# Performance work log

Hardware: AMD Instinct MI355X
Metric: run time of the kernel (lower is better)

The kernel has to match this reference:

```python
import jax, jax.numpy as jnp
import numpy as np

E, H, L = 512, 1024, 4
VS, VT = 32000, 32000
B, SS, TT = 64, 48, 48
PAD = 0


def _cell(x, h, c, Wih, Whh, bih, bhh):
    # torch.nn.LSTMCell math: gate order i, f, g, o
    g = x @ Wih.T + h @ Whh.T + bih + bhh
    i, f, gg, o = jnp.split(g, 4, axis=-1)
    c = jax.nn.sigmoid(f) * c + jax.nn.sigmoid(i) * jnp.tanh(gg)
    h = jax.nn.sigmoid(o) * jnp.tanh(c)
    return h, c


def setup_inputs() -> dict:
    key = jax.random.key(0)
    ks = jax.random.split(key, 14)
    s = 0.05
    d = {}
    d['src_tokens'] = jax.random.randint(ks[0], (SS, B), 0, VS, dtype=jnp.int32)
    d['tgt_tokens'] = jax.random.randint(ks[1], (TT, B), 0, VT, dtype=jnp.int32)
    d['src_emb'] = jax.random.normal(ks[2], (VS, E)) * s
    d['tgt_emb'] = jax.random.normal(ks[3], (VT, E)) * s
    d['enc_Wih0'] = jax.random.normal(ks[4], (4 * H, E)) * s
    d['enc_WihR'] = jax.random.normal(ks[5], (L - 1, 4 * H, H)) * s
    d['enc_Whh'] = jax.random.normal(ks[6], (L, 4 * H, H)) * s
    d['enc_bih'] = jnp.zeros((L, 4 * H))
    d['enc_bhh'] = jnp.zeros((L, 4 * H))
    d['dec_Wih0'] = jax.random.normal(ks[7], (4 * H, E + H)) * s
    d['dec_WihR'] = jax.random.normal(ks[8], (L - 1, 4 * H, H)) * s
    d['dec_Whh'] = jax.random.normal(ks[9], (L, 4 * H, H)) * s
    d['dec_bih'] = jnp.zeros((L, 4 * H))
    d['dec_bhh'] = jnp.zeros((L, 4 * H))
    d['att_vec_W'] = jax.random.normal(ks[10], (H, 2 * H)) * s
    d['readout_W'] = jax.random.normal(ks[11], (VT, H)) * s
    return d


def _forward(src_tokens, tgt_tokens, src_emb, tgt_emb, enc_Wih0, enc_WihR,
             enc_Whh, enc_bih, enc_bhh, dec_Wih0, dec_WihR, dec_Whh, dec_bih,
             dec_bhh, att_vec_W, readout_W):
    src_x = src_emb[src_tokens]                      # [SS, B, E]
    h0 = jnp.zeros((L, B, H), src_emb.dtype)
    c0 = jnp.zeros((L, B, H), src_emb.dtype)

    def enc_step(carry, x_t):
        h, c = carry
        inp = x_t
        hs, cs = [], []
        for l in range(L):
            Wih = enc_Wih0 if l == 0 else enc_WihR[l - 1]
            hn, cn = _cell(inp, h[l], c[l], Wih, enc_Whh[l], enc_bih[l], enc_bhh[l])
            hs.append(hn); cs.append(cn)
            inp = hn
        return (jnp.stack(hs), jnp.stack(cs)), inp

    (hT, cT), enc_out = jax.lax.scan(enc_step, (h0, c0), src_x)
    src_enc = enc_out.transpose(1, 0, 2)             # [B, SS, H]

    # decoder init: last encoder layer (h, c) copied to every decoder layer
    hd = jnp.tile(hT[-1][None], (L, 1, 1))
    cd = jnp.tile(cT[-1][None], (L, 1, 1))
    tgt_x = tgt_emb[tgt_tokens[:-1]]                 # [TT-1, B, E]
    att0 = jnp.zeros((B, H), src_emb.dtype)

    def dec_step(carry, y_t):
        h, c, att = carry
        inp = jnp.concatenate([y_t, att], axis=-1)   # input feeding
        hs, cs = [], []
        for l in range(L):
            Wih = dec_Wih0 if l == 0 else dec_WihR[l - 1]
            hn, cn = _cell(inp, h[l], c[l], Wih, dec_Whh[l], dec_bih[l], dec_bhh[l])
            hs.append(hn); cs.append(cn)
            inp = hn
        h_top = hs[-1]
        # global attention, 'dot' score (full-length seqs -> all-zero mask is a no-op)
        scores = jnp.einsum('bsh,bh->bs', src_enc, h_top)
        alpha = jax.nn.softmax(scores, axis=-1)
        ctx = jnp.einsum('bs,bsh->bh', alpha, src_enc)
        att_t = jnp.tanh(jnp.concatenate([h_top, ctx], axis=-1) @ att_vec_W.T)
        return (jnp.stack(hs), jnp.stack(cs), att_t), att_t

    _, att_ves = jax.lax.scan(dec_step, (hd, cd, att0), tgt_x)  # [TT-1, B, H]

    logp = jax.nn.log_softmax(att_ves @ readout_W.T, axis=-1)   # [TT-1, B, VT]
    gold = tgt_tokens[1:]
    gold_lp = jnp.take_along_axis(logp, gold[..., None], axis=-1)[..., 0]
    mask = (gold != PAD).astype(logp.dtype)
    return (gold_lp * mask).sum(axis=0)              # [B]


def reference(src_tokens, tgt_tokens, src_emb, tgt_emb, enc_Wih0, enc_WihR,
              enc_Whh, enc_bih, enc_bhh, dec_Wih0, dec_WihR, dec_Whh, dec_bih,
              dec_bhh, att_vec_W, readout_W):
    return _forward(src_tokens, tgt_tokens, src_emb, tgt_emb, enc_Wih0,
                    enc_WihR, enc_Whh, enc_bih, enc_bhh, dec_Wih0, dec_WihR,
                    dec_Whh, dec_bih, dec_bhh, att_vec_W, readout_W)
```

## Files before the change

### kernel.cpp

```cpp
#include <hip/hip_runtime.h>


typedef __attribute__((ext_vector_type(8))) short bf16x8;
typedef __attribute__((ext_vector_type(4))) float f32x4;

#define SMEM_G  49152
#define SMEM_A  65536
#define SMEM_R  40960

#define NMT_SYNC_LIGHT()                                   \
  do {                                                     \
    asm volatile("s_waitcnt lgkmcnt(0)" ::: "memory");     \
    __builtin_amdgcn_s_barrier();                          \
    __builtin_amdgcn_sched_barrier(0);                     \
  } while (0)

__device__ __forceinline__ float bf2f(ushort u) {
  union { uint i; float f; } v; v.i = ((uint)u) << 16; return v.f;
}
__device__ __forceinline__ ushort f2bf(float x) {
  union { float f; uint i; } v; v.f = x;
  uint r = (v.i + 0x7fffu + ((v.i >> 16) & 1u)) >> 16;
  return (ushort)r;
}
__device__ __forceinline__ uint pack2(float x, float y) {
  return (uint)f2bf(x) | ((uint)f2bf(y) << 16);
}
__device__ __forceinline__ float sigm(float x) {
  return __fdividef(1.f, 1.f + __expf(-x));
}
__device__ __forceinline__ float tanhf_fast(float x) {
  const float e = __expf(2.f * x);
  return 1.f - __fdividef(2.f, e + 1.f);
}

__device__ __forceinline__ void gemm_term(
    const ushort* __restrict__ A, int lda,
    const ushort* __restrict__ W, int ldw,
    int K, int m0, int n0,
    f32x4 acc[4], char* s)
{
  const int tid = threadIdx.x;
  const int lane = tid & 63;
  const int w = tid >> 6;
  const int r0 = tid >> 3;
  const int cge = (tid & 7) << 3;
  const int so0 = r0 * 128 + (((tid & 7) << 4) ^ ((r0 & 7) << 4));
  const ushort* Ar0 = A + (size_t)(m0 + r0) * lda + cge;
  const ushort* Ar1 = A + (size_t)(m0 + r0 + 32) * lda + cge;
  const ushort* Wr0 = W + (size_t)(n0 + r0) * ldw + cge;
  const ushort* Wr1 = W + (size_t)(n0 + r0 + 32) * ldw + cge;
  const int NT = K >> 6;

  uint4 a0s0, a1s0, b0s0, b1s0;
  uint4 a0s1, a1s1, b0s1, b1s1;
  uint4 a0s2, a1s2, b0s2, b1s2;

  a0s0 = *(const uint4*)(Ar0);       a1s0 = *(const uint4*)(Ar1);
  b0s0 = *(const uint4*)(Wr0);       b1s0 = *(const uint4*)(Wr1);
  a0s1 = *(const uint4*)(Ar0 + 64);  a1s1 = *(const uint4*)(Ar1 + 64);
  b0s1 = *(const uint4*)(Wr0 + 64);  b1s1 = *(const uint4*)(Wr1 + 64);
  a0s2 = *(const uint4*)(Ar0 + 128); a1s2 = *(const uint4*)(Ar1 + 128);
  b0s2 = *(const uint4*)(Wr0 + 128); b1s2 = *(const uint4*)(Wr1 + 128);
  {
    char* sl = s;
    *(uint4*)(sl + so0) = a0s0;         *(uint4*)(sl + 4096 + so0) = a1s0;
    *(uint4*)(sl + 8192 + so0) = b0s0;  *(uint4*)(sl + 12288 + so0) = b1s0;
    sl = s + 16384;
    *(uint4*)(sl + so0) = a0s1;         *(uint4*)(sl + 4096 + so0) = a1s1;
    *(uint4*)(sl + 8192 + so0) = b0s1;  *(uint4*)(sl + 12288 + so0) = b1s1;
  }
  if (3 < NT) {
    a0s0 = *(const uint4*)(Ar0 + 192); a1s0 = *(const uint4*)(Ar1 + 192);
    b0s0 = *(const uint4*)(Wr0 + 192); b1s0 = *(const uint4*)(Wr1 + 192);
  }
  if (4 < NT) {
    a0s1 = *(const uint4*)(Ar0 + 256); a1s1 = *(const uint4*)(Ar1 + 256);
    b0s1 = *(const uint4*)(Wr0 + 256); b1s1 = *(const uint4*)(Wr1 + 256);
  }

  const int axor = (lane & 7) << 4;
  const int arow = (w * 16 + (lane & 15)) * 128;
  const int brow = (lane & 15) * 128;
  const int kb0 = (lane >> 4) << 4;

#define NMT_ROUND(KR, CUR, ST)                                                \
  do {                                                                        \
    NMT_SYNC_LIGHT();                                                         \
    if ((KR) + 2 < NT) {                                                      \
      char* sl_ = s + (ST) * 16384;                                           \
      *(uint4*)(sl_ + so0) = a0s##ST;                                         \
      *(uint4*)(sl_ + 4096 + so0) = a1s##ST;                                  \
      *(uint4*)(sl_ + 8192 + so0) = b0s##ST;                                  \
      *(uint4*)(sl_ + 12288 + so0) = b1s##ST;                                 \
      if ((KR) + 5 < NT) {                                                    \
        const int off_ = ((KR) + 5) << 6;                                     \
        a0s##ST = *(const uint4*)(Ar0 + off_);                                \
        a1s##ST = *(const uint4*)(Ar1 + off_);                                \
        b0s##ST = *(const uint4*)(Wr0 + off_);                                \
        b1s##ST = *(const uint4*)(Wr1 + off_);                                \
      }                                                                       \
    }                                                                         \
    char* cur_ = s + (CUR) * 16384;                                           \
    _Pragma("unroll")                                                         \
    for (int ks = 0; ks < 2; ++ks) {                                          \
      const int kb = (ks << 6) + kb0;                                         \
      bf16x8 af = *(const bf16x8*)(cur_ + arow + (kb ^ axor));                \
      _Pragma("unroll")                                                       \
      for (int nf = 0; nf < 4; ++nf) {                                        \
        bf16x8 bfr = *(const bf16x8*)(cur_ + 8192 + nf * 2048 + brow +        \
                                      (kb ^ axor));                           \
        acc[nf] = __builtin_amdgcn_mfma_f32_16x16x32_bf16(af, bfr, acc[nf],   \
                                                          0, 0, 0);           \
      }                                                                       \
    }                                                                         \
  } while (0)

  for (int kb_ = 0; kb_ < NT; kb_ += 3) {
    NMT_ROUND(kb_ + 0, 0, 2);
    if (kb_ + 1 < NT) NMT_ROUND(kb_ + 1, 1, 0);
    if (kb_ + 2 < NT) NMT_ROUND(kb_ + 2, 2, 1);
  }
#undef NMT_ROUND
  __syncthreads();
}

__device__ __forceinline__ void att_loadf(
    const float* H0, const float* H1, const float* C0, const float* C1,
    int kt, float4* fh, float4* fc)
{
#pragma unroll
  for (int q = 0; q < 8; ++q) {
    const int rh = q >> 2, sub = (q >> 1) & 1, vq = q & 1;
    const float* hp_ = rh ? H1 : H0;
    const float* cp_ = rh ? C1 : C0;
    fh[q] = *reinterpret_cast<const float4*>(hp_ + kt + sub * 64 + vq * 4);
    fc[q] = *reinterpret_cast<const float4*>(cp_ + kt + sub * 64 + vq * 4);
  }
}

__device__ __forceinline__ void att_store(
    char* buf, int soX, const float4* fh, const float4* fc)
{
#pragma unroll
  for (int rh = 0; rh < 2; ++rh)
#pragma unroll
    for (int sub = 0; sub < 2; ++sub) {
      const int q0 = rh * 4 + sub * 2;
      const float4 u = fh[q0], v = fc[q0];
      const float4 u2 = fh[q0 + 1], v2 = fc[q0 + 1];
      uint4 o;
      o.x = pack2(tanhf_fast(u.x + v.x), tanhf_fast(u.y + v.y));
      o.y = pack2(tanhf_fast(u.z + v.z), tanhf_fast(u.w + v.w));
      o.z = pack2(tanhf_fast(u2.x + v2.x), tanhf_fast(u2.y + v2.y));
      o.w = pack2(tanhf_fast(u2.z + v2.z), tanhf_fast(u2.w + v2.w));
      *reinterpret_cast<uint4*>(buf + sub * 8192 + rh * 4096 + soX) = o;
    }
}

__device__ __forceinline__ void gemm_att(
    const float* __restrict__ H, const float* __restrict__ C2,
    const ushort* __restrict__ W, int ldw, int n0,
    f32x4 acc[4], char* s)
{
  char* sA0 = s;
  char* sB0 = s + 16384;
  char* sA1 = s + 32768;
  char* sB1 = s + 49152;
  const int tid = threadIdx.x;
  const int lane = tid & 63;
  const int w = tid >> 6;
  const int r0 = tid >> 3;
  const int cge = (tid & 7) << 3;
  const int soX = r0 * 128 + (((tid & 7) << 4) ^ ((r0 & 7) << 4));
  const ushort* Wr0 = W + (size_t)(n0 + r0) * ldw + cge;
  const ushort* Wr1 = W + (size_t)(n0 + r0 + 32) * ldw + cge;
  const float* H0 = H + r0 * 1024 + cge;
  const float* H1 = H + (r0 + 32) * 1024 + cge;
  const float* C0 = C2 + r0 * 1024 + cge;
  const float* C1 = C2 + (r0 + 32) * 1024 + cge;

  float4 fh[8], fc[8];
  uint4 b0, b1, b2, b3;
  att_loadf(H0, H1, C0, C1, 0, fh, fc);
  att_store(sA0, soX, fh, fc);
  b0 = *reinterpret_cast<const uint4*>(Wr0);
  b1 = *reinterpret_cast<const uint4*>(Wr1);
  b2 = *reinterpret_cast<const uint4*>(Wr0 + 64);
  b3 = *reinterpret_cast<const uint4*>(Wr1 + 64);
  *reinterpret_cast<uint4*>(sB0 + soX) = b0;
  *reinterpret_cast<uint4*>(sB0 + 4096 + soX) = b1;
  *reinterpret_cast<uint4*>(sB0 + 8192 + soX) = b2;
  *reinterpret_cast<uint4*>(sB0 + 12288 + soX) = b3;
  att_loadf(H0, H1, C0, C1, 128, fh, fc);
  b0 = *reinterpret_cast<const uint4*>(Wr0 + 128);
  b1 = *reinterpret_cast<const uint4*>(Wr1 + 128);
  b2 = *reinterpret_cast<const uint4*>(Wr0 + 192);
  b3 = *reinterpret_cast<const uint4*>(Wr1 + 192);

  const int axor = (lane & 7) << 4;
  const int arow = (w * 16 + (lane & 15)) * 128;
  const int brow = (lane & 15) * 128;
  const int kb0 = (lane >> 4) << 4;
  for (int kt = 0; kt < 1024; kt += 128) {
    char* cA = (kt & 128) ? sA1 : sA0;
    char* cB = (kt & 128) ? sB1 : sB0;
    char* nA = (kt & 128) ? sA0 : sA1;
    char* nB = (kt & 128) ? sB0 : sB1;
    NMT_SYNC_LIGHT();
    if (kt + 128 < 1024) {
      att_store(nA, soX, fh, fc);
      *reinterpret_cast<uint4*>(nB + soX) = b0;
      *reinterpret_cast<uint4*>(nB + 4096 + soX) = b1;
      *reinterpret_cast<uint4*>(nB + 8192 + soX) = b2;
      *reinterpret_cast<uint4*>(nB + 12288 + soX) = b3;
      if (kt + 256 < 1024) {
        att_loadf(H0, H1, C0, C1, kt + 256, fh, fc);
        b0 = *reinterpret_cast<const uint4*>(Wr0 + kt + 256);
        b1 = *reinterpret_cast<const uint4*>(Wr1 + kt + 256);
        b2 = *reinterpret_cast<const uint4*>(Wr0 + kt + 320);
        b3 = *reinterpret_cast<const uint4*>(Wr1 + kt + 320);
      }
    }
#pragma unroll
    for (int ks = 0; ks < 4; ++ks) {
      const int sb = (ks >> 1) * 8192;
      const int kb = ((ks & 1) << 6) + kb0;
      bf16x8 af = *reinterpret_cast<const bf16x8*>(cA + sb + arow + (kb ^ axor));
#pragma unroll
      for (int nf = 0; nf < 4; ++nf) {
        bf16x8 bfr = *reinterpret_cast<const bf16x8*>(
            cB + sb + nf * 2048 + brow + (kb ^ axor));
        acc[nf] = __builtin_amdgcn_mfma_f32_16x16x32_bf16(af, bfr, acc[nf], 0, 0, 0);
      }
    }
  }
  __syncthreads();
}

__device__ __forceinline__ void store_f32(
    float* __restrict__ out, int ldo, int m0, int n0, f32x4 acc[4])
{
  const int tid = threadIdx.x, lane = tid & 63, w = tid >> 6;
  const int rbase = w * 16 + ((lane >> 4) << 2);
  const int cb = lane & 15;
#pragma unroll
  for (int nf = 0; nf < 4; ++nf)
#pragma unroll
    for (int r = 0; r < 4; ++r)
      out[(size_t)(m0 + rbase + r) * ldo + n0 + nf * 16 + cb] = acc[nf][r];
}

__device__ __forceinline__ void cell_store(
    float* smemF, f32x4 acc[4],
    float* __restrict__ c, ushort* __restrict__ hout,
    ushort* __restrict__ senc_t, int j0)
{
  const int tid = threadIdx.x, lane = tid & 63, w = tid >> 6;
  const int rbase = w * 16 + ((lane >> 4) << 2);
  const int cb = lane & 15;
  __syncthreads();
#pragma unroll
  for (int nf = 0; nf < 4; ++nf)
#pragma unroll
    for (int r = 0; r < 4; ++r)
      smemF[(rbase + r) * 68 + nf * 16 + cb] = acc[nf][r];
  __syncthreads();
#pragma unroll
  for (int i = 0; i < 4; ++i) {
    const int id = tid + i * 256;
    const int b = id >> 4, u = id & 15;
    const float g0 = smemF[b * 68 + u * 4 + 0];
    const float g1 = smemF[b * 68 + u * 4 + 1];
    const float g2 = smemF[b * 68 + u * 4 + 2];
    const float g3 = smemF[b * 68 + u * 4 + 3];
    const int off = b * 1024 + j0 + u;
    const float cold = c[off];
    const float cn = sigm(g1) * cold + sigm(g0) * tanhf_fast(g2);
    const float hv = sigm(g3) * tanhf_fast(cn);
    c[off] = cn;
    const ushort hb = f2bf(hv);
    hout[off] = hb;
    if (senc_t) senc_t[(size_t)b * 49152 + j0 + u] = hb;
  }
}

__global__ __launch_bounds__(256) void nmt_init(
    float* c, ushort* henc, float* hbAll, float* ctxAll)
{
  const int idx = blockIdx.x * 256 + threadIdx.x;
  if (idx < 262144) c[idx] = 0.f;
  if (idx < 65536) {
    hbAll[idx] = 0.f;
    ctxAll[idx] = 0.f;
    henc[idx] = 0;
    henc[(size_t)1 * 49 * 65536 + idx] = 0;
    henc[(size_t)2 * 49 * 65536 + idx] = 0;
    henc[(size_t)3 * 49 * 65536 + idx] = 0;
  }
}

__global__ __launch_bounds__(256) void nmt_convperm(
    const float* __restrict__ in, ushort* __restrict__ out,
    int L, int Kin, int col0, int Kout)
{
  const size_t idx = (size_t)blockIdx.x * 256 + threadIdx.x;
  const size_t total = (size_t)L * 4096 * Kout;
  if (idx >= total) return;
  const int k = (int)(idx % Kout);
  const size_t rem = idx / Kout;
  const int rp = (int)(rem % 4096);
  const int l = (int)(rem / 4096);
  const int j = rp >> 2, g = rp & 3;
  out[idx] = f2bf(in[((size_t)l * 4096 + g * 1024 + j) * Kin + col0 + k]);
}

__global__ __launch_bounds__(256) void nmt_convplain(
    const float* __restrict__ in, ushort* __restrict__ out, size_t n)
{
  const size_t idx = (size_t)blockIdx.x * 256 + threadIdx.x;
  if (idx < n) out[idx] = f2bf(in[idx]);
}

__global__ __launch_bounds__(256) void nmt_bias(
    const float* __restrict__ bih, const float* __restrict__ bhh, float* __restrict__ bc)
{
  const int idx = blockIdx.x * 256 + threadIdx.x;
  if (idx >= 4 * 4096) return;
  const int rp = idx & 4095, l = idx >> 12;
  const int j = rp >> 2, g = rp & 3;
  bc[idx] = bih[l * 4096 + g * 1024 + j] + bhh[l * 4096 + g * 1024 + j];
}

__global__ __launch_bounds__(256) void nmt_gather(
    const int* __restrict__ tok, const float* __restrict__ emb,
    ushort* __restrict__ out, int rows)
{
  const size_t idx = (size_t)blockIdx.x * 256 + threadIdx.x;
  if (idx >= (size_t)rows * 512) return;
  const int k = (int)(idx & 511);
  const int r = (int)(idx >> 9);
  out[idx] = f2bf(emb[(size_t)tok[r] * 512 + k]);
}

__global__ __launch_bounds__(256) void nmt_pre(
    const ushort* __restrict__ A, const ushort* __restrict__ Wp,
    const float* __restrict__ bc0, float* __restrict__ out, int K)
{
  __shared__ __align__(16) char smem[SMEM_G];
  const int m0 = blockIdx.x * 64, n0 = blockIdx.y * 64;
  const int lane = threadIdx.x & 63;
  const int cb = lane & 15;
  f32x4 acc[4];
#pragma unroll
  for (int nf = 0; nf < 4; ++nf) {
    const float bv = bc0[n0 + nf * 16 + cb];
#pragma unroll
    for (int r = 0; r < 4; ++r) acc[nf][r] = bv;
  }
  gemm_term(A, K, Wp, K, K, m0, n0, acc, smem);
  store_f32(out, 4096, m0, n0, acc);
}

__global__ __launch_bounds__(256) void nmt_decinit(
    const ushort* __restrict__ henc, float* c, ushort* h)
{
  const int idx = blockIdx.x * 256 + threadIdx.x;
  if (idx >= 65536) return;
  const ushort hv = henc[((size_t)3 * 49 + 48) * 65536 + idx];
  const float cv = c[3 * 65536 + idx];
  c[idx] = cv; c[65536 + idx] = cv; c[2 * 65536 + idx] = cv;
  h[idx] = hv; h[65536 + idx] = hv; h[2 * 65536 + idx] = hv; h[3 * 65536 + idx] = hv;
}

__global__ __launch_bounds__(256) void nmt_sv(
    const ushort* __restrict__ senc, const ushort* __restrict__ attW,
    ushort* __restrict__ SV)
{
  __shared__ __align__(16) char smem[SMEM_G];
  const int b = blockIdx.x;
  const int n0 = blockIdx.y * 64;
  const int tid = threadIdx.x, lane = tid & 63, w = tid >> 6;
  const int rbase = w * 16 + ((lane >> 4) << 2), cb = lane & 15;
  f32x4 acc[4];
#pragma unroll
  for (int nf = 0; nf < 4; ++nf)
#pragma unroll
    for (int r = 0; r < 4; ++r) acc[nf][r] = 0.f;
  gemm_term(senc + (size_t)b * 49152, 1024, attW + 1024, 2048, 1024, 0, n0,
            acc, smem);
#pragma unroll
  for (int nf = 0; nf < 4; ++nf)
#pragma unroll
    for (int r = 0; r < 4; ++r) {
      const int row = rbase + r;
      if (row < 48)
        SV[(size_t)b * 49152 + row * 1024 + n0 + nf * 16 + cb] = f2bf(acc[nf][r]);
    }
}

__global__ __launch_bounds__(256) void nmt_enc_cell(
    int u, int lo, ushort* __restrict__ henc, ushort* __restrict__ srcenc,
    float* __restrict__ c,
    const ushort* __restrict__ WihR, const ushort* __restrict__ Whh,
    const float* __restrict__ X0, const float* __restrict__ bcE)
{
  __shared__ __align__(16) char smem[SMEM_G];
  const int l = lo + blockIdx.y;
  const int t = u - l;
  const int n0 = blockIdx.x * 64;
  const int tid = threadIdx.x, lane = tid & 63, w = tid >> 6;
  const int rbase = w * 16 + ((lane >> 4) << 2), cb = lane & 15;
  f32x4 acc[4];
  if (l == 0) {
#pragma unroll
    for (int nf = 0; nf < 4; ++nf)
#pragma unroll
      for (int r = 0; r < 4; ++r)
        acc[nf][r] = X0[(size_t)t * 262144 + (size_t)(rbase + r) * 4096 + n0 + nf * 16 + cb];
  } else {
#pragma unroll
    for (int nf = 0; nf < 4; ++nf) {
      const float bv = bcE[l * 4096 + n0 + nf * 16 + cb];
#pragma unroll
      for (int r = 0; r < 4; ++r) acc[nf][r] = bv;
    }
    gemm_term(henc + ((size_t)(l - 1) * 49 + t + 1) * 65536, 1024,
              WihR + (size_t)(l - 1) * 4194304, 1024, 1024, 0, n0, acc, smem);
  }
  gemm_term(henc + ((size_t)l * 49 + t) * 65536, 1024,
            Whh + (size_t)l * 4194304, 1024, 1024, 0, n0, acc, smem);
  cell_store((float*)smem, acc, c + l * 65536,
             henc + ((size_t)l * 49 + t + 1) * 65536,
             (l == 3) ? (srcenc + t * 1024) : (ushort*)nullptr, n0 >> 2);
}

__global__ __launch_bounds__(256) void nmt_dec_stage(
    int l, const ushort* __restrict__ hp, ushort* __restrict__ hn,
    float* __restrict__ c,
    const ushort* __restrict__ Whh, const ushort* __restrict__ WihR,
    const ushort* __restrict__ Wd0a,
    const float* __restrict__ hbprev, const float* __restrict__ ctxprev,
    const float* __restrict__ Y0t, const float* __restrict__ bcD,
    float* __restrict__ pbuf)
{
  __shared__ __align__(16) char smem[SMEM_A];
  const int n0 = blockIdx.x * 64;
  const int tid = threadIdx.x, lane = tid & 63, w = tid >> 6;
  const int rbase = w * 16 + ((lane >> 4) << 2), cb = lane & 15;
  f32x4 acc[4];
  if (blockIdx.y == 0) {
    if (l == 0) {
#pragma unroll
      for (int nf = 0; nf < 4; ++nf)
#pragma unroll
        for (int r = 0; r < 4; ++r) {
          const size_t o = (size_t)(rbase + r) * 4096 + n0 + nf * 16 + cb;
          acc[nf][r] = Y0t[o] + pbuf[o];
        }
      gemm_att(hbprev, ctxprev, Wd0a, 1024, n0, acc, smem);
    } else {
#pragma unroll
      for (int nf = 0; nf < 4; ++nf)
#pragma unroll
        for (int r = 0; r < 4; ++r)
          acc[nf][r] = pbuf[(size_t)l * 262144 + (size_t)(rbase + r) * 4096 + n0 + nf * 16 + cb];
      gemm_term(hn + (l - 1) * 65536, 1024, WihR + (size_t)(l - 1) * 4194304,
                1024, 1024, 0, n0, acc, smem);
    }
    cell_store((float*)smem, acc, c + l * 65536, hn + l * 65536,
               (ushort*)nullptr, n0 >> 2);
  } else {
    const int lp = (l + 1) & 3;
    if (lp == 0) {
#pragma unroll
      for (int nf = 0; nf < 4; ++nf)
#pragma unroll
        for (int r = 0; r < 4; ++r) acc[nf][r] = 0.f;
      gemm_term(hn, 1024, Whh, 1024, 1024, 0, n0, acc, smem);
    } else {
#pragma unroll
      for (int nf = 0; nf < 4; ++nf) {
        const float bv = bcD[lp * 4096 + n0 + nf * 16 + cb];
#pragma unroll
        for (int r = 0; r < 4; ++r) acc[nf][r] = bv;
      }
      gemm_term(hp + lp * 65536, 1024, Whh + (size_t)lp * 4194304,
                1024, 1024, 0, n0, acc, smem);
    }
    store_f32(pbuf + (size_t)lp * 262144, 4096, 0, n0, acc);
  }
}

__global__ __launch_bounds__(256) void nmt_partial0(
    const ushort* __restrict__ h0, const ushort* __restrict__ Whh0,
    float* __restrict__ pbuf)
{
  __shared__ __align__(16) char smem[SMEM_G];
  const int n0 = blockIdx.x * 64;
  f32x4 acc[4];
#pragma unroll
  for (int nf = 0; nf < 4; ++nf)
#pragma unroll
    for (int r = 0; r < 4; ++r) acc[nf][r] = 0.f;
  gemm_term(h0, 1024, Whh0, 1024, 1024, 0, n0, acc, smem);
  store_f32(pbuf, 4096, 0, n0, acc);
}

__global__ __launch_bounds__(256) void nmt_attnAB(
    const ushort* __restrict__ h3, const ushort* __restrict__ senc,
    const ushort* __restrict__ SV, const ushort* __restrict__ attW,
    float* __restrict__ ctx2, float* __restrict__ hb)
{
  __shared__ __align__(16) char smem[SMEM_G];
  const int bid = blockIdx.x;
  const int tid = threadIdx.x, lane = tid & 63, w = tid >> 6;
  if (bid < 64) {
    float* sc = (float*)smem;
    float* al = (float*)smem + 64;
    const int b = bid;
    const ushort* sb = senc + (size_t)b * 49152;
    const ushort* vb = SV + (size_t)b * 49152;
    float hreg[16];
#pragma unroll
    for (int q = 0; q < 16; ++q) hreg[q] = bf2f(h3[b * 1024 + lane * 16 + q]);
    for (int s = w; s < 48; s += 4) {
      const ushort* vr = sb + s * 1024 + lane * 16;
      float p = 0.f;
#pragma unroll
      for (int q = 0; q < 16; ++q) p += bf2f(vr[q]) * hreg[q];
      for (int d = 1; d < 64; d <<= 1) p += __shfl_xor(p, d);
      if (lane == 0) sc[s] = p;
    }
    __syncthreads();
    if (tid < 64) {
      const float v = (lane < 48) ? sc[lane] : -3.4e38f;
      float m = v;
      for (int d = 1; d < 64; d <<= 1) m = fmaxf(m, __shfl_xor(m, d));
      float e = (lane < 48) ? expf(v - m) : 0.f;
      float s = e;
      for (int d = 1; d < 64; d <<= 1) s += __shfl_xor(s, d);
      al[lane] = e / s;
    }
    __syncthreads();
    const int k0 = tid * 4;
    float a0 = 0, a1 = 0, a2 = 0, a3 = 0;
    for (int s = 0; s < 48; ++s) {
      const float als = al[s];
      const ushort* vr = vb + s * 1024 + k0;
      a0 += als * bf2f(vr[0]); a1 += als * bf2f(vr[1]);
      a2 += als * bf2f(vr[2]); a3 += als * bf2f(vr[3]);
    }
    ctx2[b * 1024 + k0 + 0] = a0; ctx2[b * 1024 + k0 + 1] = a1;
    ctx2[b * 1024 + k0 + 2] = a2; ctx2[b * 1024 + k0 + 3] = a3;
  } else {
    const int n0 = (bid - 64) * 64;
    f32x4 acc[4];
#pragma unroll
    for (int nf = 0; nf < 4; ++nf)
#pragma unroll
      for (int r = 0; r < 4; ++r) acc[nf][r] = 0.f;
    gemm_term(h3, 1024, attW, 2048, 1024, 0, n0, acc, smem);
    store_f32(hb, 1024, 0, n0, acc);
  }
}

__global__ __launch_bounds__(256) void nmt_attves_k(
    const float* __restrict__ hbAll, const float* __restrict__ ctxAll,
    ushort* __restrict__ attves)
{
  const int i = blockIdx.x * 1024 + threadIdx.x * 4;
#pragma unroll
  for (int k = 0; k < 4; ++k) {
    const int j = i + k;
    attves[j] = f2bf(tanhf_fast(hbAll[j + 65536] + ctxAll[j + 65536]));
  }
}

__global__ __launch_bounds__(256) void nmt_readout(
    const ushort* __restrict__ attves, const ushort* __restrict__ routW,
    const int* __restrict__ tgt, float* __restrict__ pmax,
    float* __restrict__ psum, float* __restrict__ goldl)
{
  __shared__ __align__(16) char smem[SMEM_R];
  const int g = blockIdx.x;
  const int n0 = blockIdx.y * 64;
  const int tid = threadIdx.x, lane = tid & 63, w = tid >> 6;
  const int rbase = w * 16 + ((lane >> 4) << 2), cb = lane & 15;
  const int r0 = tid >> 3;
  const int cge = (tid & 7) << 3;
  const int soX = r0 * 128 + (((tid & 7) << 4) ^ ((r0 & 7) << 4));
  const int axor = (lane & 7) << 4;
  const int arow = (w * 16 + (lane & 15)) * 128;
  const int brow = (lane & 15) * 128;
  const int kb0 = (lane >> 4) << 4;

  f32x4 acc[4][4];
#pragma unroll
  for (int mi = 0; mi < 4; ++mi)
#pragma unroll
    for (int nf = 0; nf < 4; ++nf)
#pragma unroll
      for (int r = 0; r < 4; ++r) acc[mi][nf][r] = 0.f;

  for (int kt = 0; kt < 1024; kt += 64) {
    __syncthreads();
#pragma unroll
    for (int mi = 0; mi < 4; ++mi) {
      const size_t mr = (size_t)(g * 256 + mi * 64 + r0) * 1024 + kt + cge;
      *(uint4*)(smem + mi * 8192 + soX) = *(const uint4*)(attves + mr);
      *(uint4*)(smem + mi * 8192 + 4096 + soX) = *(const uint4*)(attves + mr + 32 * 1024);
    }
    {
      const size_t wr = (size_t)(n0 + r0) * 1024 + kt + cge;
      *(uint4*)(smem + 32768 + soX) = *(const uint4*)(routW + wr);
      *(uint4*)(smem + 32768 + 4096 + soX) = *(const uint4*)(routW + wr + 32 * 1024);
    }
    __syncthreads();
#pragma unroll
    for (int ks = 0; ks < 2; ++ks) {
      const int kb = (ks << 6) + kb0;
      bf16x8 bf0 = *(const bf16x8*)(smem + 32768 + 0 * 2048 + brow + (kb ^ axor));
      bf16x8 bf1 = *(const bf16x8*)(smem + 32768 + 1 * 2048 + brow + (kb ^ axor));
      bf16x8 bf2 = *(const bf16x8*)(smem + 32768 + 2 * 2048 + brow + (kb ^ axor));
      bf16x8 bf3 = *(const bf16x8*)(smem + 32768 + 3 * 2048 + brow + (kb ^ axor));
#pragma unroll
      for (int mi = 0; mi < 4; ++mi) {
        bf16x8 af = *(const bf16x8*)(smem + mi * 8192 + arow + (kb ^ axor));
        acc[mi][0] = __builtin_amdgcn_mfma_f32_16x16x32_bf16(af, bf0, acc[mi][0], 0, 0, 0);
        acc[mi][1] = __builtin_amdgcn_mfma_f32_16x16x32_bf16(af, bf1, acc[mi][1], 0, 0, 0);
        acc[mi][2] = __builtin_amdgcn_mfma_f32_16x16x32_bf16(af, bf2, acc[mi][2], 0, 0, 0);
        acc[mi][3] = __builtin_amdgcn_mfma_f32_16x16x32_bf16(af, bf3, acc[mi][3], 0, 0, 0);
      }
    }
  }

#pragma unroll
  for (int mi = 0; mi < 4; ++mi) {
    const int gm = g * 4 + mi;
    if (gm >= 47) continue;
#pragma unroll
    for (int r = 0; r < 4; ++r) {
      float lm = fmaxf(fmaxf(acc[mi][0][r], acc[mi][1][r]),
                       fmaxf(acc[mi][2][r], acc[mi][3][r]));
      for (int d = 1; d < 16; d <<= 1) lm = fmaxf(lm, __shfl_xor(lm, d));
      float ls = 0.f;
#pragma unroll
      for (int nf = 0; nf < 4; ++nf) ls += expf(acc[mi][nf][r] - lm);
      for (int d = 1; d < 16; d <<= 1) ls += __shfl_xor(ls, d);
      const int grow = gm * 64 + rbase + r;
      if (cb == 0) {
        pmax[(size_t)grow * 500 + blockIdx.y] = lm;
        psum[(size_t)grow * 500 + blockIdx.y] = ls;
      }
      const int t = grow >> 6, b = grow & 63;
      const int gold = tgt[(t + 1) * 64 + b];
#pragma unroll
      for (int nf = 0; nf < 4; ++nf)
        if (n0 + nf * 16 + cb == gold) goldl[grow] = acc[mi][nf][r];
    }
  }
}

__global__ __launch_bounds__(64) void nmt_combine(
    const float* __restrict__ pmax, const float* __restrict__ psum,
    const float* __restrict__ goldl, const int* __restrict__ tgt,
    float* __restrict__ lpm)
{
  const int row = blockIdx.x;
  const int lane = threadIdx.x;
  float m = -3.4e38f, s = 0.f;
  for (int i = lane; i < 500; i += 64) {
    const float pm = pmax[(size_t)row * 500 + i];
    const float ps = psum[(size_t)row * 500 + i];
    if (pm > m) { s = s * expf(m - pm) + ps; m = pm; }
    else        { s += ps * expf(pm - m); }
  }
  for (int d = 1; d < 64; d <<= 1) {
    const float om = __shfl_xor(m, d), os = __shfl_xor(s, d);
    if (om > m) { s = s * expf(m - om) + os; m = om; }
    else        { s += os * expf(om - m); }
  }
  if (lane == 0) {
    const int t = row >> 6, b = row & 63;
    const int gold = tgt[(t + 1) * 64 + b];
    const float lp = goldl[row] - m - logf(s);
    lpm[row] = (gold != 0) ? lp : 0.f;
  }
}

__global__ __launch_bounds__(64) void nmt_final(
    const float* __restrict__ lpm, float* __restrict__ out)
{
  const int b = threadIdx.x;
  float s = 0.f;
  for (int t = 0; t < 47; ++t) s += lpm[t * 64 + b];
  out[b] = s;
}

extern "C" void kernel_launch(void* const* d_in, const int* in_sizes, int n_in,
                              void* d_out, int out_size, void* d_ws, size_t ws_size,
                              hipStream_t stream)
{
  (void)in_sizes; (void)n_in; (void)out_size; (void)ws_size;
  const int*   src_tok  = (const int*)d_in[0];
  const int*   tgt_tok  = (const int*)d_in[1];
  const float* src_emb  = (const float*)d_in[2];
  const float* tgt_emb  = (const float*)d_in[3];
  const float* eWih0    = (const float*)d_in[4];
  const float* eWihR    = (const float*)d_in[5];
  const float* eWhh     = (const float*)d_in[6];
  const float* ebih     = (const float*)d_in[7];
  const float* ebhh     = (const float*)d_in[8];
  const float* dWih0    = (const float*)d_in[9];
  const float* dWihR    = (const float*)d_in[10];
  const float* dWhh     = (const float*)d_in[11];
  const float* dbih     = (const float*)d_in[12];
  const float* dbhh     = (const float*)d_in[13];
  const float* attW_f   = (const float*)d_in[14];
  const float* routW_f  = (const float*)d_in[15];

  char* p = (char*)d_ws;
  auto alloc = [&](size_t bytes) { void* r = (void*)p; p += (bytes + 255) & ~(size_t)255; return r; };
  ushort* eWih0p = (ushort*)alloc((size_t)4096 * 512 * 2);
  ushort* eWihRp = (ushort*)alloc((size_t)3 * 4096 * 1024 * 2);
  ushort* eWhhp  = (ushort*)alloc((size_t)4 * 4096 * 1024 * 2);
  ushort* dWih0y = (ushort*)alloc((size_t)4096 * 512 * 2);
  ushort* dWih0a = (ushort*)alloc((size_t)4096 * 1024 * 2);
  ushort* dWihRp = (ushort*)alloc((size_t)3 * 4096 * 1024 * 2);
  ushort* dWhhp  = (ushort*)alloc((size_t)4 * 4096 * 1024 * 2);
  ushort* attWb  = (ushort*)alloc((size_t)1024 * 2048 * 2);
  ushort* routWb = (ushort*)alloc((size_t)32000 * 1024 * 2);
  ushort* srcx   = (ushort*)alloc((size_t)3072 * 512 * 2);
  ushort* tgtx   = (ushort*)alloc((size_t)3008 * 512 * 2);
  ushort* henc   = (ushort*)alloc((size_t)4 * 49 * 65536 * 2);
  ushort* hA     = (ushort*)alloc((size_t)4 * 65536 * 2);
  ushort* hB     = (ushort*)alloc((size_t)4 * 65536 * 2);
  ushort* srcenc = (ushort*)alloc((size_t)64 * 49152 * 2);
  ushort* SVbuf  = (ushort*)alloc((size_t)64 * 49152 * 2);
  ushort* attves = (ushort*)alloc((size_t)3072 * 1024 * 2);
  float*  hbAll  = (float*)alloc((size_t)48 * 65536 * 4);
  float*  ctxAll = (float*)alloc((size_t)48 * 65536 * 4);
  float*  pbuf   = (float*)alloc((size_t)4 * 262144 * 4);
  float*  X0     = (float*)alloc((size_t)3072 * 4096 * 4);
  float*  Y0     = (float*)alloc((size_t)3008 * 4096 * 4);
  float*  bcE    = (float*)alloc((size_t)16384 * 4);
  float*  bcD    = (float*)alloc((size_t)16384 * 4);
  float*  cbuf   = (float*)alloc((size_t)4 * 65536 * 4);
  float*  pmaxb  = (float*)alloc((size_t)3008 * 500 * 4);
  float*  psumb  = (float*)alloc((size_t)3008 * 500 * 4);
  float*  goldl  = (float*)alloc((size_t)3008 * 4);
  float*  lpm    = (float*)alloc((size_t)3008 * 4);

  const dim3 B256(256);
  auto g1 = [](size_t n) { return dim3((unsigned)((n + 255) / 256)); };

  nmt_init<<<g1(262144), B256, 0, stream>>>(cbuf, henc, hbAll, ctxAll);

  nmt_convperm<<<g1((size_t)4096 * 512), B256, 0, stream>>>(eWih0, eWih0p, 1, 512, 0, 512);
  nmt_convperm<<<g1((size_t)3 * 4096 * 1024), B256, 0, stream>>>(eWihR, eWihRp, 3, 1024, 0, 1024);
  nmt_convperm<<<g1((size_t)4 * 4096 * 1024), B256, 0, stream>>>(eWhh, eWhhp, 4, 1024, 0, 1024);
  nmt_convperm<<<g1((size_t)4096 * 512), B256, 0, stream>>>(dWih0, dWih0y, 1, 1536, 0, 512);
  nmt_convperm<<<g1((size_t)4096 * 1024), B256, 0, stream>>>(dWih0, dWih0a, 1, 1536, 512, 1024);
  nmt_convperm<<<g1((size_t)3 * 4096 * 1024), B256, 0, stream>>>(dWihR, dWihRp, 3, 1024, 0, 1024);
  nmt_convperm<<<g1((size_t)4 * 4096 * 1024), B256, 0, stream>>>(dWhh, dWhhp, 4, 1024, 0, 1024);
  nmt_convplain<<<g1((size_t)1024 * 2048), B256, 0, stream>>>(attW_f, attWb, (size_t)1024 * 2048);
  nmt_convplain<<<g1((size_t)32000 * 1024), B256, 0, stream>>>(routW_f, routWb, (size_t)32000 * 1024);
  nmt_bias<<<g1(16384), B256, 0, stream>>>(ebih, ebhh, bcE);
  nmt_bias<<<g1(16384), B256, 0, stream>>>(dbih, dbhh, bcD);
  nmt_gather<<<g1((size_t)3072 * 512), B256, 0, stream>>>(src_tok, src_emb, srcx, 3072);
  nmt_gather<<<g1((size_t)3008 * 512), B256, 0, stream>>>(tgt_tok, tgt_emb, tgtx, 3008);

  nmt_pre<<<dim3(48, 64), B256, 0, stream>>>(srcx, eWih0p, bcE, X0, 512);
  nmt_pre<<<dim3(47, 64), B256, 0, stream>>>(tgtx, dWih0y, bcD, Y0, 512);

  for (int u = 0; u < 51; ++u) {
    const int lo = (u > 47) ? (u - 47) : 0;
    const int hi = (u < 3) ? u : 3;
    nmt_enc_cell<<<dim3(64, hi - lo + 1), B256, 0, stream>>>(
        u, lo, henc, srcenc, cbuf, eWihRp, eWhhp, X0, bcE);
  }
  nmt_decinit<<<g1(65536), B256, 0, stream>>>(henc, cbuf, hA);
  nmt_sv<<<dim3(64, 16), B256, 0, stream>>>(srcenc, attWb, SVbuf);
  nmt_partial0<<<dim3(64), B256, 0, stream>>>(hA, dWhhp, pbuf);

  for (int t = 0; t < 47; ++t) {
    ushort* hp = (t & 1) ? hB : hA;
    ushort* hn = (t & 1) ? hA : hB;
    for (int l = 0; l < 4; ++l) {
      nmt_dec_stage<<<dim3(64, 2), B256, 0, stream>>>(
          l, hp, hn, cbuf, dWhhp, dWihRp, dWih0a,
          hbAll + (size_t)t * 65536, ctxAll + (size_t)t * 65536,
          Y0 + (size_t)t * 262144, bcD, pbuf);
    }
    nmt_attnAB<<<dim3(80), B256, 0, stream>>>(
        hn + 3 * 65536, srcenc, SVbuf, attWb,
        ctxAll + (size_t)(t + 1) * 65536, hbAll + (size_t)(t + 1) * 65536);
  }
  nmt_attves_k<<<dim3(3008), B256, 0, stream>>>(hbAll, ctxAll, attves);

  nmt_readout<<<dim3(12, 500), B256, 0, stream>>>(attves, routWb, tgt_tok,
                                                  pmaxb, psumb, goldl);
  nmt_combine<<<dim3(3008), dim3(64), 0, stream>>>(pmaxb, psumb, goldl, tgt_tok, lpm);
  nmt_final<<<dim3(1), dim3(64), 0, stream>>>(lpm, (float*)d_out);
}
```

Before: 4.498 ms.

## Split encoder cell into pipelined input/recurrent halves and enlarge readout M tile

The encoder wavefront is restructured so each layer's input-projection GEMM (WihR·h_below) runs one tick ahead as a separate block set, writing partial sums to a new buffer. The cell blocks then only do the recurrent Whh GEMM plus the cell update, which shortens each launch's critical path at the cost of more ticks (54 instead of 51) and extra fp32 partial-sum traffic. Separately, the readout GEMM tile doubles along M (8 row groups per block, 6 instead of 12 blocks in x) to reuse each loaded weight tile across more rows. This raises shared memory to 72KB and doubles the accumulator registers, which may lower occupancy.

```diff
diff --git a/kernel.cpp b/kernel.cpp
--- a/kernel.cpp
+++ b/kernel.cpp
@@ -6,7 +6,7 @@
 
 #define SMEM_G  49152
 #define SMEM_A  65536
-#define SMEM_R  40960
+#define SMEM_R  73728
 
 #define NMT_SYNC_LIGHT()                                   \
   do {                                                     \
@@ -399,40 +399,53 @@
     }
 }
 
-__global__ __launch_bounds__(256) void nmt_enc_cell(
-    int u, int lo, ushort* __restrict__ henc, ushort* __restrict__ srcenc,
+__global__ __launch_bounds__(256) void nmt_enc_tick(
+    int v, int lc0, int ncell, int lp0,
+    ushort* __restrict__ henc, ushort* __restrict__ srcenc,
     float* __restrict__ c,
     const ushort* __restrict__ WihR, const ushort* __restrict__ Whh,
-    const float* __restrict__ X0, const float* __restrict__ bcE)
+    const float* __restrict__ X0, const float* __restrict__ bcE,
+    float* __restrict__ pbufE)
 {
   __shared__ __align__(16) char smem[SMEM_G];
-  const int l = lo + blockIdx.y;
-  const int t = u - l;
   const int n0 = blockIdx.x * 64;
   const int tid = threadIdx.x, lane = tid & 63, w = tid >> 6;
   const int rbase = w * 16 + ((lane >> 4) << 2), cb = lane & 15;
   f32x4 acc[4];
-  if (l == 0) {
-#pragma unroll
-    for (int nf = 0; nf < 4; ++nf)
-#pragma unroll
-      for (int r = 0; r < 4; ++r)
-        acc[nf][r] = X0[(size_t)t * 262144 + (size_t)(rbase + r) * 4096 + n0 + nf * 16 + cb];
+  if ((int)blockIdx.y < ncell) {
+    const int l = lc0 + blockIdx.y;
+    const int t = v - 2 * l;
+    if (l == 0) {
+#pragma unroll
+      for (int nf = 0; nf < 4; ++nf)
+#pragma unroll
+        for (int r = 0; r < 4; ++r)
+          acc[nf][r] = X0[(size_t)t * 262144 + (size_t)(rbase + r) * 4096 + n0 + nf * 16 + cb];
+    } else {
+#pragma unroll
+      for (int nf = 0; nf < 4; ++nf)
+#pragma unroll
+        for (int r = 0; r < 4; ++r)
+          acc[nf][r] = pbufE[(size_t)l * 262144 + (size_t)(rbase + r) * 4096 + n0 + nf * 16 + cb];
+    }
+    gemm_term(henc + ((size_t)l * 49 + t) * 65536, 1024,
+              Whh + (size_t)l * 4194304, 1024, 1024, 0, n0, acc, smem);
+    cell_store((float*)smem, acc, c + l * 65536,
+               henc + ((size_t)l * 49 + t + 1) * 65536,
+               (l == 3) ? (srcenc + t * 1024) : (ushort*)nullptr, n0 >> 2);
   } else {
+    const int l = lp0 + (blockIdx.y - ncell);
+    const int tp = v + 1 - 2 * l;
 #pragma unroll
     for (int nf = 0; nf < 4; ++nf) {
       const float bv = bcE[l * 4096 + n0 + nf * 16 + cb];
 #pragma unroll
       for (int r = 0; r < 4; ++r) acc[nf][r] = bv;
     }
-    gemm_term(henc + ((size_t)(l - 1) * 49 + t + 1) * 65536, 1024,
+    gemm_term(henc + ((size_t)(l - 1) * 49 + tp + 1) * 65536, 1024,
               WihR + (size_t)(l - 1) * 4194304, 1024, 1024, 0, n0, acc, smem);
-  }
-  gemm_term(henc + ((size_t)l * 49 + t) * 65536, 1024,
-            Whh + (size_t)l * 4194304, 1024, 1024, 0, n0, acc, smem);
-  cell_store((float*)smem, acc, c + l * 65536,
-             henc + ((size_t)l * 49 + t + 1) * 65536,
-             (l == 3) ? (srcenc + t * 1024) : (ushort*)nullptr, n0 >> 2);
+    store_f32(pbufE + (size_t)l * 262144, 4096, 0, n0, acc);
+  }
 }
 
 __global__ __launch_bounds__(256) void nmt_dec_stage(
@@ -595,9 +608,9 @@
   const int brow = (lane & 15) * 128;
   const int kb0 = (lane >> 4) << 4;
 
-  f32x4 acc[4][4];
-#pragma unroll
-  for (int mi = 0; mi < 4; ++mi)
+  f32x4 acc[8][4];
+#pragma unroll
+  for (int mi = 0; mi < 8; ++mi)
 #pragma unroll
     for (int nf = 0; nf < 4; ++nf)
 #pragma unroll
@@ -606,26 +619,26 @@
   for (int kt = 0; kt < 1024; kt += 64) {
     __syncthreads();
 #pragma unroll
-    for (int mi = 0; mi < 4; ++mi) {
-      const size_t mr = (size_t)(g * 256 + mi * 64 + r0) * 1024 + kt + cge;
+    for (int mi = 0; mi < 8; ++mi) {
+      const size_t mr = (size_t)(g * 512 + mi * 64 + r0) * 1024 + kt + cge;
       *(uint4*)(smem + mi * 8192 + soX) = *(const uint4*)(attves + mr);
       *(uint4*)(smem + mi * 8192 + 4096 + soX) = *(const uint4*)(attves + mr + 32 * 1024);
     }
     {
       const size_t wr = (size_t)(n0 + r0) * 1024 + kt + cge;
-      *(uint4*)(smem + 32768 + soX) = *(const uint4*)(routW + wr);
-      *(uint4*)(smem + 32768 + 4096 + soX) = *(const uint4*)(routW + wr + 32 * 1024);
+      *(uint4*)(smem + 65536 + soX) = *(const uint4*)(routW + wr);
+      *(uint4*)(smem + 65536 + 4096 + soX) = *(const uint4*)(routW + wr + 32 * 1024);
     }
     __syncthreads();
 #pragma unroll
     for (int ks = 0; ks < 2; ++ks) {
       const int kb = (ks << 6) + kb0;
-      bf16x8 bf0 = *(const bf16x8*)(smem + 32768 + 0 * 2048 + brow + (kb ^ axor));
-      bf16x8 bf1 = *(const bf16x8*)(smem + 32768 + 1 * 2048 + brow + (kb ^ axor));
-      bf16x8 bf2 = *(const bf16x8*)(smem + 32768 + 2 * 2048 + brow + (kb ^ axor));
-      bf16x8 bf3 = *(const bf16x8*)(smem + 32768 + 3 * 2048 + brow + (kb ^ axor));
-#pragma unroll
-      for (int mi = 0; mi < 4; ++mi) {
+      bf16x8 bf0 = *(const bf16x8*)(smem + 65536 + 0 * 2048 + brow + (kb ^ axor));
+      bf16x8 bf1 = *(const bf16x8*)(smem + 65536 + 1 * 2048 + brow + (kb ^ axor));
+      bf16x8 bf2 = *(const bf16x8*)(smem + 65536 + 2 * 2048 + brow + (kb ^ axor));
+      bf16x8 bf3 = *(const bf16x8*)(smem + 65536 + 3 * 2048 + brow + (kb ^ axor));
+#pragma unroll
+      for (int mi = 0; mi < 8; ++mi) {
         bf16x8 af = *(const bf16x8*)(smem + mi * 8192 + arow + (kb ^ axor));
         acc[mi][0] = __builtin_amdgcn_mfma_f32_16x16x32_bf16(af, bf0, acc[mi][0], 0, 0, 0);
         acc[mi][1] = __builtin_amdgcn_mfma_f32_16x16x32_bf16(af, bf1, acc[mi][1], 0, 0, 0);
@@ -636,8 +649,8 @@
   }
 
 #pragma unroll
-  for (int mi = 0; mi < 4; ++mi) {
-    const int gm = g * 4 + mi;
+  for (int mi = 0; mi < 8; ++mi) {
+    const int gm = g * 8 + mi;
     if (gm >= 47) continue;
 #pragma unroll
     for (int r = 0; r < 4; ++r) {
@@ -742,6 +755,7 @@
   float*  hbAll  = (float*)alloc((size_t)48 * 65536 * 4);
   float*  ctxAll = (float*)alloc((size_t)48 * 65536 * 4);
   float*  pbuf   = (float*)alloc((size_t)4 * 262144 * 4);
+  float*  pbufE  = (float*)alloc((size_t)4 * 262144 * 4);
   float*  X0     = (float*)alloc((size_t)3072 * 4096 * 4);
   float*  Y0     = (float*)alloc((size_t)3008 * 4096 * 4);
   float*  bcE    = (float*)alloc((size_t)16384 * 4);
@@ -774,11 +788,16 @@
   nmt_pre<<<dim3(48, 64), B256, 0, stream>>>(srcx, eWih0p, bcE, X0, 512);
   nmt_pre<<<dim3(47, 64), B256, 0, stream>>>(tgtx, dWih0y, bcD, Y0, 512);
 
-  for (int u = 0; u < 51; ++u) {
-    const int lo = (u > 47) ? (u - 47) : 0;
-    const int hi = (u < 3) ? u : 3;
-    nmt_enc_cell<<<dim3(64, hi - lo + 1), B256, 0, stream>>>(
-        u, lo, henc, srcenc, cbuf, eWihRp, eWhhp, X0, bcE);
+  for (int v = 0; v < 54; ++v) {
+    int lc0 = (v > 47) ? ((v - 47 + 1) / 2) : 0;
+    int lc1 = (v / 2 < 3) ? (v / 2) : 3;
+    int ncell = lc1 - lc0 + 1;
+    int lp0 = (v + 1 > 47) ? ((v + 1 - 47 + 1) / 2) : 1;
+    if (lp0 < 1) lp0 = 1;
+    int lp1 = ((v + 1) / 2 < 3) ? ((v + 1) / 2) : 3;
+    int npart = (lp1 >= lp0) ? (lp1 - lp0 + 1) : 0;
+    nmt_enc_tick<<<dim3(64, ncell + npart), B256, 0, stream>>>(
+        v, lc0, ncell, lp0, henc, srcenc, cbuf, eWihRp, eWhhp, X0, bcE, pbufE);
   }
   nmt_decinit<<<g1(65536), B256, 0, stream>>>(henc, cbuf, hA);
   nmt_sv<<<dim3(64, 16), B256, 0, stream>>>(srcenc, attWb, SVbuf);
@@ -799,8 +818,8 @@
   }
   nmt_attves_k<<<dim3(3008), B256, 0, stream>>>(hbAll, ctxAll, attves);
 
-  nmt_readout<<<dim3(12, 500), B256, 0, stream>>>(attves, routWb, tgt_tok,
-                                                  pmaxb, psumb, goldl);
+  nmt_readout<<<dim3(6, 500), B256, 0, stream>>>(attves, routWb, tgt_tok,
+                                                 pmaxb, psumb, goldl);
   nmt_combine<<<dim3(3008), dim3(64), 0, stream>>>(pmaxb, psumb, goldl, tgt_tok, lpm);
   nmt_final<<<dim3(1), dim3(64), 0, stream>>>(lpm, (float*)d_out);
 }
```

Measured after the change: 4.720 ms. +4.9%, slower.
